# Kernel optimization log

Measured on AMD Instinct MI355X. Metric: run time of the kernel, lower is better.

The kernel has to match this reference:

```python
import jax, jax.numpy as jnp
import numpy as np

N = 32768          # nodes
E = 524288         # edges (avg degree 16)
H = 128            # hidden_features
EF = 16            # edge_features
MF = 2 * H + EF + 1  # message_features for e3, relaxed=False (distance feat = 1)


def _mlp2(x, W1, b1, W2, b2):
    # Linear -> silu -> Linear -> silu (edge_mlp)
    return jax.nn.silu(jax.nn.silu(x @ W1 + b1) @ W2 + b2)


def setup_inputs() -> dict:
    key = jax.random.key(0)
    ks = jax.random.split(key, 20)

    def glorot(k, shape):
        fan_in, fan_out = shape[0], shape[1]
        lim = np.sqrt(6.0 / (fan_in + fan_out)).astype(np.float32)
        return jax.random.uniform(k, shape, jnp.float32, -lim, lim)

    inp = {
        'src': jax.random.randint(ks[0], (E,), 0, N),
        'dst': jax.random.randint(ks[1], (E,), 0, N),
        'h': jax.random.normal(ks[2], (N, H), jnp.float32),
        'coords': jax.random.normal(ks[3], (N, 3), jnp.float32),
        'a': jax.random.normal(ks[4], (E, EF), jnp.float32),
        # coord_mlp: MF -> H -> H -> 1 (last bias-free, xavier gain 0.001)
        'W_c1': glorot(ks[5], (MF, H)), 'b_c1': jnp.zeros((H,), jnp.float32),
        'W_c2': glorot(ks[6], (H, H)),  'b_c2': jnp.zeros((H,), jnp.float32),
        'W_c3': glorot(ks[7], (H, 1)) * 0.001,
        # edge_mlp: MF -> H -> H
        'W_e1': glorot(ks[8], (MF, H)), 'b_e1': jnp.zeros((H,), jnp.float32),
        'W_e2': glorot(ks[9], (H, H)),  'b_e2': jnp.zeros((H,), jnp.float32),
        # att_mlp: H -> 1
        'W_att': glorot(ks[10], (H, 1)), 'b_att': jnp.zeros((1,), jnp.float32),
        # node_mlp: 2H -> H -> H
        'W_n1': glorot(ks[11], (2 * H, H)), 'b_n1': jnp.zeros((H,), jnp.float32),
        'W_n2': glorot(ks[12], (H, H)),     'b_n2': jnp.zeros((H,), jnp.float32),
    }
    return inp


def reference(src, dst, h, coords, a,
              W_c1, b_c1, W_c2, b_c2, W_c3,
              W_e1, b_e1, W_e2, b_e2,
              W_att, b_att,
              W_n1, b_n1, W_n2, b_n2):
    # --- edge gather + distance features (equivariance='e3', relaxed=False) ---
    srcs_x = coords[src]                      # [E, 3]
    dsts_x = coords[dst]
    diffs = srcs_x - dsts_x                   # [E, 3]
    radials = jnp.sum(diffs * diffs, axis=-1, keepdims=True)  # [E, 1]

    f = jnp.concatenate([h[src], h[dst], radials, a], axis=-1)  # [E, MF]

    # --- coord messages ---
    c = jax.nn.silu(f @ W_c1 + b_c1)
    c = jax.nn.silu(c @ W_c2 + b_c2)
    scale = c @ W_c3                          # [E, 1]
    msg_x = scale * diffs / (jnp.sqrt(radials + 1e-05) + 1.0)   # [E, 3]

    # --- hidden messages with attention gating ---
    msg_h = _mlp2(f, W_e1, b_e1, W_e2, b_e2)  # [E, H]
    att = jax.nn.sigmoid(msg_h @ W_att + b_att)  # [E, 1]
    msg_h = att * msg_h

    # --- scatter-sum aggregation at destination nodes ---
    x_agg = jax.ops.segment_sum(msg_x, dst, num_segments=N)  # [N, 3]
    h_agg = jax.ops.segment_sum(msg_h, dst, num_segments=N)  # [N, H]

    coords_out = coords + x_agg
    nh = jax.nn.silu(jnp.concatenate([h, h_agg], axis=-1) @ W_n1 + b_n1) @ W_n2 + b_n2
    h_out = h + nh
    return (h_out, coords_out)
```

## Files before the change

### kernel.cpp

```cpp
#include <hip/hip_runtime.h>
#include <math.h>

#define HD   128
#define EFD  16
#define MT   64
#define LPA  264
#define LPC  136

#define W1SZ (128 * 288)
#define W2SZ (128 * 128)
#define O_WE1 (W1SZ)
#define O_WC2 (2 * W1SZ)
#define O_WE2 (2 * W1SZ + W2SZ)
#define O_WN1 (2 * W1SZ + 2 * W2SZ)
#define O_WN2 (2 * W1SZ + 2 * W2SZ + 128 * 256)
#define WS_ELEMS (O_WN2 + W2SZ)

#define B_H16   ((size_t)0)
#define B_WPAN  ((size_t)8388608)
#define B_CNT   ((size_t)8699904)
#define B_OFS   ((size_t)8830976)
#define B_SRCP  ((size_t)8962048)
#define B_DSTP  ((size_t)11059200)
#define B_A16   ((size_t)13156352)

typedef __attribute__((ext_vector_type(8))) short short8;
typedef __attribute__((ext_vector_type(4))) float f32x4;

__device__ __forceinline__ unsigned short f2bf(float x) {
    __bf16 b = (__bf16)x;
    unsigned short u;
    __builtin_memcpy(&u, &b, 2);
    return u;
}
__device__ __forceinline__ float bf2f(unsigned short u) {
    union { unsigned u; float f; } v; v.u = ((unsigned)u) << 16;
    return v.f;
}
__device__ __forceinline__ float sigm_f(float x) {
    return __builtin_amdgcn_rcpf(1.f + __expf(-x));
}
__device__ __forceinline__ float silu_f(float x) { return x * sigm_f(x); }
__device__ __forceinline__ unsigned pack2(float a, float b) {
    return (unsigned)f2bf(a) | ((unsigned)f2bf(b) << 16);
}

__device__ __forceinline__ void frag_l1(int idx, const float* __restrict__ W,
                                        const float* __restrict__ bias,
                                        unsigned short* __restrict__ out)
{
    const int j = idx & 7, lane = (idx >> 3) & 63, blk = idx >> 9;
    const int kc = blk % 9, n = blk / 9;
    const int k = kc * 32 + (lane >> 4) * 8 + j;
    const int c = n * 16 + (lane & 15);
    float v = 0.f;
    if (k < 256) v = W[k * HD + c];
    else if (k < 272) v = W[(k + 1) * HD + c];
    else if (k == 272) v = W[256 * HD + c];
    else if (k == 273) v = bias[c];
    out[idx] = f2bf(v);
}
__device__ __forceinline__ void frag_sq(int idx, const float* __restrict__ W,
                                        int nkc, unsigned short* __restrict__ out)
{
    const int j = idx & 7, lane = (idx >> 3) & 63, blk = idx >> 9;
    const int kc = blk % nkc, n = blk / nkc;
    const int k = kc * 32 + (lane >> 4) * 8 + j;
    const int c = n * 16 + (lane & 15);
    out[idx] = f2bf(W[k * HD + c]);
}

__global__ __launch_bounds__(256) void fused_prep(
    const float* __restrict__ h, unsigned short* __restrict__ h16,
    const float* __restrict__ Wc1, const float* __restrict__ bc1,
    const float* __restrict__ We1, const float* __restrict__ be1,
    const float* __restrict__ Wc2, const float* __restrict__ We2,
    const float* __restrict__ Wn1, const float* __restrict__ Wn2,
    unsigned short* __restrict__ ws,
    const int* __restrict__ dst, unsigned* __restrict__ cnt,
    int nConv, int nPrep, int E)
{
    const int bid = blockIdx.x, tid = threadIdx.x;
    if (bid < nConv) {
        const int i = bid * 256 + tid;
        const float4 v = ((const float4*)h)[i];
        union { unsigned short us[4]; uint2 u2; } p;
        p.us[0] = f2bf(v.x); p.us[1] = f2bf(v.y);
        p.us[2] = f2bf(v.z); p.us[3] = f2bf(v.w);
        ((uint2*)h16)[i] = p.u2;
        return;
    }
    if (bid < nConv + nPrep) {
        int idx = (bid - nConv) * 256 + tid;
        if (idx < W1SZ)            { frag_l1(idx, Wc1, bc1, ws);            return; }
        idx -= W1SZ;
        if (idx < W1SZ)            { frag_l1(idx, We1, be1, ws + O_WE1);    return; }
        idx -= W1SZ;
        if (idx < W2SZ)            { frag_sq(idx, Wc2, 4, ws + O_WC2);      return; }
        idx -= W2SZ;
        if (idx < W2SZ)            { frag_sq(idx, We2, 4, ws + O_WE2);      return; }
        idx -= W2SZ;
        if (idx < 128 * 256)       { frag_sq(idx, Wn1, 8, ws + O_WN1);      return; }
        idx -= 128 * 256;
        if (idx < W2SZ)            { frag_sq(idx, Wn2, 4, ws + O_WN2); }
        return;
    }
    const int i = (bid - nConv - nPrep) * 256 + tid;
    if (i < E) atomicAdd(&cnt[dst[i]], 1u);
}

__global__ __launch_bounds__(1024) void scan32k(const unsigned* __restrict__ cnt,
                                                unsigned* __restrict__ ofs)
{
    __shared__ unsigned wsum[16];
    __shared__ unsigned carry_s;
    const int tid = threadIdx.x, lane = tid & 63, w = tid >> 6;
    if (tid == 0) carry_s = 0;
    __syncthreads();
    for (int c = 0; c < 32; ++c) {
        const unsigned x = cnt[c * 1024 + tid];
        unsigned v = x;
        #pragma unroll
        for (int off = 1; off < 64; off <<= 1) {
            unsigned t = __shfl_up(v, off);
            if (lane >= off) v += t;
        }
        if (lane == 63) wsum[w] = v;
        __syncthreads();
        if (tid < 16) {
            unsigned s = wsum[tid];
            #pragma unroll
            for (int off = 1; off < 16; off <<= 1) {
                unsigned t = __shfl_up(s, off);
                if (tid >= off) s += t;
            }
            wsum[tid] = s;
        }
        __syncthreads();
        const unsigned carry = carry_s;
        const unsigned woff = (w == 0) ? 0u : wsum[w - 1];
        ofs[c * 1024 + tid] = carry + woff + v - x;
        __syncthreads();
        if (tid == 0) carry_s = carry + wsum[15];
        __syncthreads();
    }
}

__global__ __launch_bounds__(256) void scatter_perm(
    const int* __restrict__ src, const int* __restrict__ dst,
    const float* __restrict__ a, unsigned* __restrict__ ofs,
    int* __restrict__ srcp, int* __restrict__ dstp,
    unsigned short* __restrict__ a16p, int E)
{
    const int i = blockIdx.x * 256 + threadIdx.x;
    if (i >= E) return;
    const int d = dst[i];
    const unsigned pos = atomicAdd(&ofs[d], 1u);
    srcp[pos] = src[i];
    dstp[pos] = d;
    const float* ar = a + (size_t)i * EFD;
    union { unsigned short us[8]; short8 v; } p0, p1;
    #pragma unroll
    for (int t = 0; t < 8; ++t) { p0.us[t] = f2bf(ar[t]); p1.us[t] = f2bf(ar[8 + t]); }
    short8* dstv = (short8*)(a16p + (size_t)pos * EFD);
    dstv[0] = p0.v; dstv[1] = p1.v;
}

__global__ __launch_bounds__(256, 4) void edge_kernel(
    const int* __restrict__ srcp, const int* __restrict__ dstp,
    const unsigned short* __restrict__ a16p,
    const float* __restrict__ coords, const unsigned short* __restrict__ h16,
    const float* __restrict__ bc2, const float* __restrict__ Wc3,
    const float* __restrict__ be2,
    const float* __restrict__ Watt, const float* __restrict__ batt,
    const unsigned short* __restrict__ wpan,
    float* __restrict__ out_h, float* __restrict__ out_x)
{
    __shared__ __align__(16) unsigned short csh_c[MT][LPC];
    __shared__ __align__(16) unsigned short csh_e[MT][LPC];
    __shared__ float diff_s[MT][3];
    __shared__ float rinv_s[MT];
    __shared__ float rad_s[MT];
    __shared__ float sc_part[4][MT];
    __shared__ float pa_part[4][MT];
    __shared__ float att_s[MT];
    __shared__ float sc_s[MT];
    __shared__ int   src_s[MT], dst_s[MT];
    __shared__ short run_start[MT + 1];
    __shared__ int   nruns_s;

    const int tid = threadIdx.x;
    const int e0  = blockIdx.x * MT;

    if (tid < MT) {
        const int s = srcp[e0 + tid], d = dstp[e0 + tid];
        src_s[tid] = s; dst_s[tid] = d;
        const float dx = coords[(size_t)s*3+0] - coords[(size_t)d*3+0];
        const float dy = coords[(size_t)s*3+1] - coords[(size_t)d*3+1];
        const float dz = coords[(size_t)s*3+2] - coords[(size_t)d*3+2];
        diff_s[tid][0] = dx; diff_s[tid][1] = dy; diff_s[tid][2] = dz;
        const float rad = dx*dx + dy*dy + dz*dz;
        rad_s[tid]  = rad;
        rinv_s[tid] = __builtin_amdgcn_rcpf(sqrtf(rad + 1e-5f) + 1.f);
    }
    __syncthreads();

    if (tid < 64) {
        const bool st = (tid == 0) || (dst_s[tid] != dst_s[tid - 1]);
        unsigned long long m = __ballot(st);
        if (tid == 0) {
            int nr = 0;
            while (m) { run_start[nr++] = (short)__builtin_ctzll(m); m &= m - 1; }
            run_start[nr] = MT;
            nruns_s = nr;
        }
    }

    const int lane = tid & 63;
    const int w    = tid >> 6;
    const int w2   = w * 2;
    const int col  = lane & 15;
    const int kg   = lane >> 4;

    const unsigned short* Wc1p = wpan            + lane * 8;
    const unsigned short* We1p = wpan + O_WE1    + lane * 8;
    const unsigned short* Wc2p = wpan + O_WC2    + lane * 8;
    const unsigned short* We2p = wpan + O_WE2    + lane * 8;

    const unsigned short* hs[4];
    const unsigned short* hd[4];
    #pragma unroll
    for (int et = 0; et < 4; ++et) {
        const int r = et * 16 + col;
        hs[et] = h16 + (size_t)src_s[r] * HD;
        hd[et] = h16 + (size_t)dst_s[r] * HD;
    }

    const f32x4 zero = {0.f, 0.f, 0.f, 0.f};
    const short8 zf  = {0,0,0,0,0,0,0,0};
    f32x4 ac[2][4], ae[2][4];

    #pragma unroll
    for (int m = 0; m < 2; ++m)
        #pragma unroll
        for (int et = 0; et < 4; ++et) { ac[m][et] = zero; ae[m][et] = zero; }

    #pragma unroll
    for (int kc = 0; kc < 9; ++kc) {
        short8 df[4];
        #pragma unroll
        for (int et = 0; et < 4; ++et) {
            if (kc < 4)       df[et] = *(const short8*)(hs[et] + kc * 32 + kg * 8);
            else if (kc < 8)  df[et] = *(const short8*)(hd[et] + (kc - 4) * 32 + kg * 8);
            else if (kg < 2)  df[et] = *(const short8*)(a16p + (size_t)(e0 + et*16 + col) * EFD + kg * 8);
            else if (kg == 2) {
                df[et] = zf;
                df[et][0] = (short)f2bf(rad_s[et*16 + col]);
                df[et][1] = (short)0x3F80;
            } else df[et] = zf;
        }
        #pragma unroll
        for (int m = 0; m < 2; ++m) {
            const short8 wc = *(const short8*)&Wc1p[((w2 + m) * 9 + kc) << 9];
            const short8 we = *(const short8*)&We1p[((w2 + m) * 9 + kc) << 9];
            #pragma unroll
            for (int et = 0; et < 4; ++et) {
                ac[m][et] = __builtin_amdgcn_mfma_f32_16x16x32_bf16(wc, df[et], ac[m][et], 0, 0, 0);
                ae[m][et] = __builtin_amdgcn_mfma_f32_16x16x32_bf16(we, df[et], ae[m][et], 0, 0, 0);
            }
        }
    }
    #pragma unroll
    for (int m = 0; m < 2; ++m)
        #pragma unroll
        for (int et = 0; et < 4; ++et) {
            const int row = et * 16 + col;
            const int hw  = w * 32 + m * 16 + kg * 4;
            uint2 vc, ve;
            vc.x = pack2(silu_f(ac[m][et][0]), silu_f(ac[m][et][1]));
            vc.y = pack2(silu_f(ac[m][et][2]), silu_f(ac[m][et][3]));
            ve.x = pack2(silu_f(ae[m][et][0]), silu_f(ae[m][et][1]));
            ve.y = pack2(silu_f(ae[m][et][2]), silu_f(ae[m][et][3]));
            *(uint2*)&csh_c[row][hw] = vc;
            *(uint2*)&csh_e[row][hw] = ve;
        }
    __syncthreads();

    #pragma unroll
    for (int m = 0; m < 2; ++m)
        #pragma unroll
        for (int et = 0; et < 4; ++et) { ac[m][et] = zero; ae[m][et] = zero; }

    #pragma unroll
    for (int kc = 0; kc < 4; ++kc) {
        short8 dc[4], de[4];
        #pragma unroll
        for (int et = 0; et < 4; ++et) {
            const int row = et * 16 + col;
            dc[et] = *(const short8*)&csh_c[row][kc * 32 + kg * 8];
            de[et] = *(const short8*)&csh_e[row][kc * 32 + kg * 8];
        }
        #pragma unroll
        for (int m = 0; m < 2; ++m) {
            const short8 wc = *(const short8*)&Wc2p[((w2 + m) * 4 + kc) << 9];
            const short8 we = *(const short8*)&We2p[((w2 + m) * 4 + kc) << 9];
            #pragma unroll
            for (int et = 0; et < 4; ++et) {
                ac[m][et] = __builtin_amdgcn_mfma_f32_16x16x32_bf16(wc, dc[et], ac[m][et], 0, 0, 0);
                ae[m][et] = __builtin_amdgcn_mfma_f32_16x16x32_bf16(we, de[et], ae[m][et], 0, 0, 0);
            }
        }
    }

    {
        float sc[4] = {0.f, 0.f, 0.f, 0.f};
        #pragma unroll
        for (int m = 0; m < 2; ++m)
            #pragma unroll
            for (int i = 0; i < 4; ++i) {
                const int hw = w * 32 + m * 16 + kg * 4 + i;
                const float b = bc2[hw], w3 = Wc3[hw];
                #pragma unroll
                for (int et = 0; et < 4; ++et)
                    sc[et] += silu_f(ac[m][et][i] + b) * w3;
            }
        #pragma unroll
        for (int et = 0; et < 4; ++et) {
            sc[et] += __shfl_xor(sc[et], 16);
            sc[et] += __shfl_xor(sc[et], 32);
        }
        if (kg == 0) {
            #pragma unroll
            for (int et = 0; et < 4; ++et)
                sc_part[w][et * 16 + col] = sc[et];
        }
    }
    __syncthreads();

    {
        float pa[4] = {0.f, 0.f, 0.f, 0.f};
        #pragma unroll
        for (int m = 0; m < 2; ++m)
            #pragma unroll
            for (int et = 0; et < 4; ++et) {
                const int row = et * 16 + col;
                const int hw  = w * 32 + m * 16 + kg * 4;
                const float v0 = silu_f(ae[m][et][0] + be2[hw]);
                const float v1 = silu_f(ae[m][et][1] + be2[hw+1]);
                const float v2 = silu_f(ae[m][et][2] + be2[hw+2]);
                const float v3 = silu_f(ae[m][et][3] + be2[hw+3]);
                pa[et] += v0 * Watt[hw] + v1 * Watt[hw+1]
                        + v2 * Watt[hw+2] + v3 * Watt[hw+3];
                uint2 ve;
                ve.x = pack2(v0, v1);
                ve.y = pack2(v2, v3);
                *(uint2*)&csh_e[row][hw] = ve;
            }
        #pragma unroll
        for (int et = 0; et < 4; ++et) {
            pa[et] += __shfl_xor(pa[et], 16);
            pa[et] += __shfl_xor(pa[et], 32);
        }
        if (kg == 0) {
            #pragma unroll
            for (int et = 0; et < 4; ++et)
                pa_part[w][et * 16 + col] = pa[et];
        }
    }
    __syncthreads();

    if (tid < MT) {
        att_s[tid] = sigm_f(pa_part[0][tid] + pa_part[1][tid] +
                            pa_part[2][tid] + pa_part[3][tid] + batt[0]);
        sc_s[tid]  = (sc_part[0][tid] + sc_part[1][tid] +
                      sc_part[2][tid] + sc_part[3][tid]) * rinv_s[tid];
    }
    __syncthreads();

    {
        const int nr    = nruns_s;
        const int colx2 = tid & 63;
        for (int r = tid >> 6; r < nr; r += 4) {
            const int s0 = run_start[r], s1 = run_start[r + 1];
            float sum0 = 0.f, sum1 = 0.f;
            for (int e = s0; e < s1; ++e) {
                const unsigned uv = *(const unsigned*)&csh_e[e][colx2 * 2];
                const float at = att_s[e];
                sum0 += bf2f((unsigned short)uv) * at;
                sum1 += bf2f((unsigned short)(uv >> 16)) * at;
            }
            const int drow = dst_s[s0];
            float* op = out_h + (size_t)drow * HD + colx2 * 2;
            atomicAdd(op,     sum0);
            atomicAdd(op + 1, sum1);
            if (colx2 < 2) {
                float sx0 = 0.f, sx1 = 0.f;
                for (int e = s0; e < s1; ++e) {
                    const float s = sc_s[e];
                    sx0 += s * diff_s[e][colx2 * 2];
                    if (colx2 == 0) sx1 += s * diff_s[e][1];
                }
                atomicAdd(&out_x[(size_t)drow * 3 + colx2 * 2], sx0);
                if (colx2 == 0) atomicAdd(&out_x[(size_t)drow * 3 + 1], sx1);
            }
        }
    }
}

__global__ __launch_bounds__(256) void node_kernel(
    const float* __restrict__ h, const float* __restrict__ coords,
    const float* __restrict__ bn1, const float* __restrict__ bn2,
    const unsigned short* __restrict__ wpan,
    float* __restrict__ out_h, float* __restrict__ out_x)
{
    __shared__ __align__(16) unsigned short ash[MT][LPA];
    __shared__ __align__(16) unsigned short csh[MT][LPC];

    const int tid = threadIdx.x;
    const int n0  = blockIdx.x * MT;

    #pragma unroll
    for (int it = 0; it < 16; ++it) {
        const int idx = it * 256 + tid;
        const int e = idx >> 6, q = idx & 63;
        const float* base = (q < 32)
            ? h     + (size_t)(n0 + e) * HD + q * 4
            : out_h + (size_t)(n0 + e) * HD + (q - 32) * 4;
        const float4 v = *(const float4*)base;
        union { unsigned short us[4]; uint2 u2; } p;
        p.us[0] = f2bf(v.x); p.us[1] = f2bf(v.y);
        p.us[2] = f2bf(v.z); p.us[3] = f2bf(v.w);
        *(uint2*)&ash[e][q * 4] = p.u2;
    }
    __syncthreads();

    if (tid < MT * 3) {
        const int n = tid / 3, d = tid % 3;
        const size_t gi = (size_t)(n0 + n) * 3 + d;
        out_x[gi] += coords[gi];
    }

    const int lane = tid & 63;
    const int w    = tid >> 6;
    const int er0  = w * 16;
    const int col  = lane & 15;
    const int kg   = lane >> 4;

    const unsigned short* Wn1p = wpan + O_WN1 + lane * 8;
    const unsigned short* Wn2p = wpan + O_WN2 + lane * 8;

    const f32x4 zero = {0.f, 0.f, 0.f, 0.f};
    f32x4 acc[8];

    #pragma unroll
    for (int n = 0; n < 8; ++n) acc[n] = zero;
    #pragma unroll
    for (int kc = 0; kc < 8; ++kc) {
        const short8 af = *(const short8*)&ash[er0 + col][kc * 32 + kg * 8];
        #pragma unroll
        for (int n = 0; n < 8; ++n) {
            const short8 bf = *(const short8*)&Wn1p[(n * 8 + kc) << 9];
            acc[n] = __builtin_amdgcn_mfma_f32_16x16x32_bf16(af, bf, acc[n], 0, 0, 0);
        }
    }
    #pragma unroll
    for (int n = 0; n < 8; ++n) {
        const float b = bn1[n*16 + col];
        #pragma unroll
        for (int i = 0; i < 4; ++i)
            csh[er0 + kg*4 + i][n*16 + col] = f2bf(silu_f(acc[n][i] + b));
    }
    __syncthreads();
    #pragma unroll
    for (int n = 0; n < 8; ++n) acc[n] = zero;
    #pragma unroll
    for (int kc = 0; kc < 4; ++kc) {
        const short8 af = *(const short8*)&csh[er0 + col][kc * 32 + kg * 8];
        #pragma unroll
        for (int n = 0; n < 8; ++n) {
            const short8 bf = *(const short8*)&Wn2p[(n * 4 + kc) << 9];
            acc[n] = __builtin_amdgcn_mfma_f32_16x16x32_bf16(af, bf, acc[n], 0, 0, 0);
        }
    }
    #pragma unroll
    for (int i = 0; i < 4; ++i) {
        const int node = n0 + er0 + kg*4 + i;
        const float* hr   = h     + (size_t)node * HD;
        float*       orow = out_h + (size_t)node * HD;
        #pragma unroll
        for (int n = 0; n < 8; ++n) {
            const int f = n*16 + col;
            orow[f] = hr[f] + acc[n][i] + bn2[f];
        }
    }
}

extern "C" void kernel_launch(void* const* d_in, const int* in_sizes, int n_in,
                              void* d_out, int out_size, void* d_ws, size_t ws_size,
                              hipStream_t stream)
{
    const int*   src    = (const int*)  d_in[0];
    const int*   dst    = (const int*)  d_in[1];
    const float* h      = (const float*)d_in[2];
    const float* coords = (const float*)d_in[3];
    const float* a      = (const float*)d_in[4];
    const float* Wc1    = (const float*)d_in[5];
    const float* bc1    = (const float*)d_in[6];
    const float* Wc2    = (const float*)d_in[7];
    const float* bc2    = (const float*)d_in[8];
    const float* Wc3    = (const float*)d_in[9];
    const float* We1    = (const float*)d_in[10];
    const float* be1    = (const float*)d_in[11];
    const float* We2    = (const float*)d_in[12];
    const float* be2    = (const float*)d_in[13];
    const float* Watt   = (const float*)d_in[14];
    const float* batt   = (const float*)d_in[15];
    const float* Wn1    = (const float*)d_in[16];
    const float* bn1    = (const float*)d_in[17];
    const float* Wn2    = (const float*)d_in[18];
    const float* bn2    = (const float*)d_in[19];

    const int E = in_sizes[0];
    const int N = in_sizes[2] / HD;

    float* out_h = (float*)d_out;
    float* out_x = out_h + (size_t)N * HD;

    char* wsb = (char*)d_ws;
    unsigned short* h16  = (unsigned short*)(wsb + B_H16);
    unsigned short* wpan = (unsigned short*)(wsb + B_WPAN);
    unsigned*       cnt  = (unsigned*)      (wsb + B_CNT);
    unsigned*       ofs  = (unsigned*)      (wsb + B_OFS);
    int*            srcp = (int*)           (wsb + B_SRCP);
    int*            dstp = (int*)           (wsb + B_DSTP);
    unsigned short* a16p = (unsigned short*)(wsb + B_A16);

    hipMemsetAsync(d_out, 0, (size_t)out_size * sizeof(float), stream);
    hipMemsetAsync(cnt, 0, (size_t)N * sizeof(unsigned), stream);

    const int nConv = (N * HD / 4) / 256;
    const int nPrep = WS_ELEMS / 256;
    const int nHist = (E + 255) / 256;

    fused_prep<<<dim3(nConv + nPrep + nHist), dim3(256), 0, stream>>>(
        h, h16, Wc1, bc1, We1, be1, Wc2, We2, Wn1, Wn2, wpan,
        dst, cnt, nConv, nPrep, E);

    scan32k<<<dim3(1), dim3(1024), 0, stream>>>(cnt, ofs);
    scatter_perm<<<dim3((E + 255) / 256), dim3(256), 0, stream>>>(
        src, dst, a, ofs, srcp, dstp, a16p, E);

    edge_kernel<<<dim3(E / MT), dim3(256), 0, stream>>>(
        srcp, dstp, a16p, coords, h16,
        bc2, Wc3, be2, Watt, batt,
        wpan, out_h, out_x);

    node_kernel<<<dim3(N / MT), dim3(256), 0, stream>>>(
        h, coords, bn1, bn2, wpan, out_h, out_x);
}
```

Measured before the change: 324.3 us.

## Precompute per-node first-layer projections and gather them per edge

Splits the first edge/coord MLP layer algebraically: h[src]@W_src and h[dst]@W_dst are computed once per node in a new node_pre kernel and stored as bf16 tables. The edge kernel then gathers and adds these partial sums instead of running eight K-chunks of MFMA on gathered h rows, keeping only the radial/edge-feature chunk. The scatter kernel now writes an edge index permutation instead of a converted a16 copy, and the edge kernel reads a directly. This trades edge-side matmul FLOPs for four extra bf16 gathers per edge. It also adds bf16 rounding of the partial sums and a larger workspace.

```diff
diff --git a/kernel.cpp b/kernel.cpp
--- a/kernel.cpp
+++ b/kernel.cpp
@@ -16,13 +16,16 @@
 #define O_WN2 (2 * W1SZ + 2 * W2SZ + 128 * 256)
 #define WS_ELEMS (O_WN2 + W2SZ)
 
-#define B_H16   ((size_t)0)
-#define B_WPAN  ((size_t)8388608)
-#define B_CNT   ((size_t)8699904)
-#define B_OFS   ((size_t)8830976)
-#define B_SRCP  ((size_t)8962048)
-#define B_DSTP  ((size_t)11059200)
-#define B_A16   ((size_t)13156352)
+#define B_PSC   ((size_t)0)
+#define B_PDC   ((size_t)8388608)
+#define B_PSE   ((size_t)16777216)
+#define B_PDE   ((size_t)25165824)
+#define B_WPAN  ((size_t)33554432)
+#define B_CNT   ((size_t)33865728)
+#define B_OFS   ((size_t)33996800)
+#define B_SRCP  ((size_t)34127872)
+#define B_DSTP  ((size_t)36225024)
+#define B_EIDX  ((size_t)38322176)
 
 typedef __attribute__((ext_vector_type(8))) short short8;
 typedef __attribute__((ext_vector_type(4))) float f32x4;
@@ -36,6 +39,12 @@
 __device__ __forceinline__ float bf2f(unsigned short u) {
     union { unsigned u; float f; } v; v.u = ((unsigned)u) << 16;
     return v.f;
+}
+__device__ __forceinline__ float bfl(unsigned u) {
+    union { unsigned u; float f; } v; v.u = u << 16; return v.f;
+}
+__device__ __forceinline__ float bfh(unsigned u) {
+    union { unsigned u; float f; } v; v.u = u & 0xffff0000u; return v.f;
 }
 __device__ __forceinline__ float sigm_f(float x) {
     return __builtin_amdgcn_rcpf(1.f + __expf(-x));
@@ -71,27 +80,17 @@
 }
 
 __global__ __launch_bounds__(256) void fused_prep(
-    const float* __restrict__ h, unsigned short* __restrict__ h16,
     const float* __restrict__ Wc1, const float* __restrict__ bc1,
     const float* __restrict__ We1, const float* __restrict__ be1,
     const float* __restrict__ Wc2, const float* __restrict__ We2,
     const float* __restrict__ Wn1, const float* __restrict__ Wn2,
     unsigned short* __restrict__ ws,
     const int* __restrict__ dst, unsigned* __restrict__ cnt,
-    int nConv, int nPrep, int E)
+    int nPrep, int E)
 {
     const int bid = blockIdx.x, tid = threadIdx.x;
-    if (bid < nConv) {
-        const int i = bid * 256 + tid;
-        const float4 v = ((const float4*)h)[i];
-        union { unsigned short us[4]; uint2 u2; } p;
-        p.us[0] = f2bf(v.x); p.us[1] = f2bf(v.y);
-        p.us[2] = f2bf(v.z); p.us[3] = f2bf(v.w);
-        ((uint2*)h16)[i] = p.u2;
-        return;
-    }
-    if (bid < nConv + nPrep) {
-        int idx = (bid - nConv) * 256 + tid;
+    if (bid < nPrep) {
+        int idx = bid * 256 + tid;
         if (idx < W1SZ)            { frag_l1(idx, Wc1, bc1, ws);            return; }
         idx -= W1SZ;
         if (idx < W1SZ)            { frag_l1(idx, We1, be1, ws + O_WE1);    return; }
@@ -105,8 +104,82 @@
         if (idx < W2SZ)            { frag_sq(idx, Wn2, 4, ws + O_WN2); }
         return;
     }
-    const int i = (bid - nConv - nPrep) * 256 + tid;
+    const int i = (bid - nPrep) * 256 + tid;
     if (i < E) atomicAdd(&cnt[dst[i]], 1u);
+}
+
+__device__ __forceinline__ void pre_pass(
+    const unsigned short* __restrict__ panelp,
+    const unsigned short* __restrict__ hsh,
+    unsigned short* __restrict__ Ps, unsigned short* __restrict__ Pd,
+    int n0, int w2, int w, int col, int kg)
+{
+    const f32x4 zero = {0.f, 0.f, 0.f, 0.f};
+    f32x4 as_[2][4], ad_[2][4];
+    #pragma unroll
+    for (int m = 0; m < 2; ++m)
+        #pragma unroll
+        for (int et = 0; et < 4; ++et) { as_[m][et] = zero; ad_[m][et] = zero; }
+    #pragma unroll
+    for (int kc = 0; kc < 4; ++kc) {
+        short8 bf[4];
+        #pragma unroll
+        for (int et = 0; et < 4; ++et)
+            bf[et] = *(const short8*)&hsh[(et*16 + col) * LPC + kc * 32 + kg * 8];
+        #pragma unroll
+        for (int m = 0; m < 2; ++m) {
+            const short8 As = *(const short8*)&panelp[((w2 + m) * 9 + kc) << 9];
+            const short8 Ad = *(const short8*)&panelp[((w2 + m) * 9 + kc + 4) << 9];
+            #pragma unroll
+            for (int et = 0; et < 4; ++et) {
+                as_[m][et] = __builtin_amdgcn_mfma_f32_16x16x32_bf16(As, bf[et], as_[m][et], 0, 0, 0);
+                ad_[m][et] = __builtin_amdgcn_mfma_f32_16x16x32_bf16(Ad, bf[et], ad_[m][et], 0, 0, 0);
+            }
+        }
+    }
+    #pragma unroll
+    for (int m = 0; m < 2; ++m)
+        #pragma unroll
+        for (int et = 0; et < 4; ++et) {
+            const size_t row = (size_t)(n0 + et * 16 + col) * HD;
+            const int hw = w * 32 + m * 16 + kg * 4;
+            uint2 vs, vd;
+            vs.x = pack2(as_[m][et][0], as_[m][et][1]);
+            vs.y = pack2(as_[m][et][2], as_[m][et][3]);
+            vd.x = pack2(ad_[m][et][0], ad_[m][et][1]);
+            vd.y = pack2(ad_[m][et][2], ad_[m][et][3]);
+            *(uint2*)(Ps + row + hw) = vs;
+            *(uint2*)(Pd + row + hw) = vd;
+        }
+}
+
+__global__ __launch_bounds__(256) void node_pre(
+    const float* __restrict__ h, const unsigned short* __restrict__ wpan,
+    unsigned short* __restrict__ Psc, unsigned short* __restrict__ Pdc,
+    unsigned short* __restrict__ Pse, unsigned short* __restrict__ Pde)
+{
+    __shared__ __align__(16) unsigned short hsh[MT][LPC];
+    const int tid = threadIdx.x;
+    const int n0  = blockIdx.x * MT;
+
+    #pragma unroll
+    for (int it = 0; it < 8; ++it) {
+        const int idx = it * 256 + tid;
+        const int r = idx >> 5, q = idx & 31;
+        const float4 v = *(const float4*)(h + (size_t)(n0 + r) * HD + q * 4);
+        uint2 p; p.x = pack2(v.x, v.y); p.y = pack2(v.z, v.w);
+        *(uint2*)&hsh[r][q * 4] = p;
+    }
+    __syncthreads();
+
+    const int lane = tid & 63;
+    const int w    = tid >> 6;
+    const int w2   = w * 2;
+    const int col  = lane & 15;
+    const int kg   = lane >> 4;
+
+    pre_pass(wpan + lane * 8,         &hsh[0][0], Psc, Pdc, n0, w2, w, col, kg);
+    pre_pass(wpan + O_WE1 + lane * 8, &hsh[0][0], Pse, Pde, n0, w2, w, col, kg);
 }
 
 __global__ __launch_bounds__(1024) void scan32k(const unsigned* __restrict__ cnt,
@@ -148,9 +221,9 @@
 
 __global__ __launch_bounds__(256) void scatter_perm(
     const int* __restrict__ src, const int* __restrict__ dst,
-    const float* __restrict__ a, unsigned* __restrict__ ofs,
+    unsigned* __restrict__ ofs,
     int* __restrict__ srcp, int* __restrict__ dstp,
-    unsigned short* __restrict__ a16p, int E)
+    int* __restrict__ eidx, int E)
 {
     const int i = blockIdx.x * 256 + threadIdx.x;
     if (i >= E) return;
@@ -158,18 +231,15 @@
     const unsigned pos = atomicAdd(&ofs[d], 1u);
     srcp[pos] = src[i];
     dstp[pos] = d;
-    const float* ar = a + (size_t)i * EFD;
-    union { unsigned short us[8]; short8 v; } p0, p1;
-    #pragma unroll
-    for (int t = 0; t < 8; ++t) { p0.us[t] = f2bf(ar[t]); p1.us[t] = f2bf(ar[8 + t]); }
-    short8* dstv = (short8*)(a16p + (size_t)pos * EFD);
-    dstv[0] = p0.v; dstv[1] = p1.v;
+    eidx[pos] = i;
 }
 
 __global__ __launch_bounds__(256, 4) void edge_kernel(
     const int* __restrict__ srcp, const int* __restrict__ dstp,
-    const unsigned short* __restrict__ a16p,
-    const float* __restrict__ coords, const unsigned short* __restrict__ h16,
+    const int* __restrict__ eidx, const float* __restrict__ a,
+    const float* __restrict__ coords,
+    const unsigned short* __restrict__ Psc, const unsigned short* __restrict__ Pdc,
+    const unsigned short* __restrict__ Pse, const unsigned short* __restrict__ Pde,
     const float* __restrict__ bc2, const float* __restrict__ Wc3,
     const float* __restrict__ be2,
     const float* __restrict__ Watt, const float* __restrict__ batt,
@@ -179,13 +249,13 @@
     __shared__ __align__(16) unsigned short csh_c[MT][LPC];
     __shared__ __align__(16) unsigned short csh_e[MT][LPC];
     __shared__ float diff_s[MT][3];
+    __shared__ float rad_s[MT];
     __shared__ float rinv_s[MT];
-    __shared__ float rad_s[MT];
     __shared__ float sc_part[4][MT];
     __shared__ float pa_part[4][MT];
     __shared__ float att_s[MT];
     __shared__ float sc_s[MT];
-    __shared__ int   src_s[MT], dst_s[MT];
+    __shared__ int   src_s[MT], dst_s[MT], eid_s[MT];
     __shared__ short run_start[MT + 1];
     __shared__ int   nruns_s;
 
@@ -195,6 +265,7 @@
     if (tid < MT) {
         const int s = srcp[e0 + tid], d = dstp[e0 + tid];
         src_s[tid] = s; dst_s[tid] = d;
+        eid_s[tid] = eidx[e0 + tid];
         const float dx = coords[(size_t)s*3+0] - coords[(size_t)d*3+0];
         const float dy = coords[(size_t)s*3+1] - coords[(size_t)d*3+1];
         const float dz = coords[(size_t)s*3+2] - coords[(size_t)d*3+2];
@@ -227,42 +298,60 @@
     const unsigned short* Wc2p = wpan + O_WC2    + lane * 8;
     const unsigned short* We2p = wpan + O_WE2    + lane * 8;
 
-    const unsigned short* hs[4];
-    const unsigned short* hd[4];
+    unsigned po_s[4], po_d[4];
     #pragma unroll
     for (int et = 0; et < 4; ++et) {
         const int r = et * 16 + col;
-        hs[et] = h16 + (size_t)src_s[r] * HD;
-        hd[et] = h16 + (size_t)dst_s[r] * HD;
-    }
-
-    const f32x4 zero = {0.f, 0.f, 0.f, 0.f};
-    const short8 zf  = {0,0,0,0,0,0,0,0};
+        const unsigned wk = (unsigned)(w * 64 + kg * 8);
+        po_s[et] = (unsigned)src_s[r] * 256u + wk;
+        po_d[et] = (unsigned)dst_s[r] * 256u + wk;
+    }
+
+    const short8 zf = {0,0,0,0,0,0,0,0};
     f32x4 ac[2][4], ae[2][4];
 
     #pragma unroll
     for (int m = 0; m < 2; ++m)
         #pragma unroll
-        for (int et = 0; et < 4; ++et) { ac[m][et] = zero; ae[m][et] = zero; }
-
-    #pragma unroll
-    for (int kc = 0; kc < 9; ++kc) {
+        for (int et = 0; et < 4; ++et) {
+            const uint2 sc_ = *(const uint2*)((const char*)Psc + po_s[et] + m * 32);
+            const uint2 dc_ = *(const uint2*)((const char*)Pdc + po_d[et] + m * 32);
+            const uint2 se_ = *(const uint2*)((const char*)Pse + po_s[et] + m * 32);
+            const uint2 de_ = *(const uint2*)((const char*)Pde + po_d[et] + m * 32);
+            ac[m][et][0] = bfl(sc_.x) + bfl(dc_.x);
+            ac[m][et][1] = bfh(sc_.x) + bfh(dc_.x);
+            ac[m][et][2] = bfl(sc_.y) + bfl(dc_.y);
+            ac[m][et][3] = bfh(sc_.y) + bfh(dc_.y);
+            ae[m][et][0] = bfl(se_.x) + bfl(de_.x);
+            ae[m][et][1] = bfh(se_.x) + bfh(de_.x);
+            ae[m][et][2] = bfl(se_.y) + bfl(de_.y);
+            ae[m][et][3] = bfh(se_.y) + bfh(de_.y);
+        }
+    {
         short8 df[4];
         #pragma unroll
         for (int et = 0; et < 4; ++et) {
-            if (kc < 4)       df[et] = *(const short8*)(hs[et] + kc * 32 + kg * 8);
-            else if (kc < 8)  df[et] = *(const short8*)(hd[et] + (kc - 4) * 32 + kg * 8);
-            else if (kg < 2)  df[et] = *(const short8*)(a16p + (size_t)(e0 + et*16 + col) * EFD + kg * 8);
-            else if (kg == 2) {
-                df[et] = zf;
-                df[et][0] = (short)f2bf(rad_s[et*16 + col]);
-                df[et][1] = (short)0x3F80;
+            if (kg < 2) {
+                const int oe = eid_s[et * 16 + col];
+                const float4 a0 = *(const float4*)(a + (size_t)oe * EFD + kg * 8);
+                const float4 a1 = *(const float4*)(a + (size_t)oe * EFD + kg * 8 + 4);
+                short8 v;
+                v[0] = (short)f2bf(a0.x); v[1] = (short)f2bf(a0.y);
+                v[2] = (short)f2bf(a0.z); v[3] = (short)f2bf(a0.w);
+                v[4] = (short)f2bf(a1.x); v[5] = (short)f2bf(a1.y);
+                v[6] = (short)f2bf(a1.z); v[7] = (short)f2bf(a1.w);
+                df[et] = v;
+            } else if (kg == 2) {
+                short8 v = zf;
+                v[0] = (short)f2bf(rad_s[et * 16 + col]);
+                v[1] = (short)0x3F80;
+                df[et] = v;
             } else df[et] = zf;
         }
         #pragma unroll
         for (int m = 0; m < 2; ++m) {
-            const short8 wc = *(const short8*)&Wc1p[((w2 + m) * 9 + kc) << 9];
-            const short8 we = *(const short8*)&We1p[((w2 + m) * 9 + kc) << 9];
+            const short8 wc = *(const short8*)&Wc1p[((w2 + m) * 9 + 8) << 9];
+            const short8 we = *(const short8*)&We1p[((w2 + m) * 9 + 8) << 9];
             #pragma unroll
             for (int et = 0; et < 4; ++et) {
                 ac[m][et] = __builtin_amdgcn_mfma_f32_16x16x32_bf16(wc, df[et], ac[m][et], 0, 0, 0);
@@ -286,6 +375,7 @@
         }
     __syncthreads();
 
+    const f32x4 zero = {0.f, 0.f, 0.f, 0.f};
     #pragma unroll
     for (int m = 0; m < 2; ++m)
         #pragma unroll
@@ -386,8 +476,8 @@
             for (int e = s0; e < s1; ++e) {
                 const unsigned uv = *(const unsigned*)&csh_e[e][colx2 * 2];
                 const float at = att_s[e];
-                sum0 += bf2f((unsigned short)uv) * at;
-                sum1 += bf2f((unsigned short)(uv >> 16)) * at;
+                sum0 += bfl(uv) * at;
+                sum1 += bfh(uv) * at;
             }
             const int drow = dst_s[s0];
             float* op = out_h + (size_t)drow * HD + colx2 * 2;
@@ -527,31 +617,37 @@
     float* out_x = out_h + (size_t)N * HD;
 
     char* wsb = (char*)d_ws;
-    unsigned short* h16  = (unsigned short*)(wsb + B_H16);
+    unsigned short* Psc  = (unsigned short*)(wsb + B_PSC);
+    unsigned short* Pdc  = (unsigned short*)(wsb + B_PDC);
+    unsigned short* Pse  = (unsigned short*)(wsb + B_PSE);
+    unsigned short* Pde  = (unsigned short*)(wsb + B_PDE);
     unsigned short* wpan = (unsigned short*)(wsb + B_WPAN);
     unsigned*       cnt  = (unsigned*)      (wsb + B_CNT);
     unsigned*       ofs  = (unsigned*)      (wsb + B_OFS);
     int*            srcp = (int*)           (wsb + B_SRCP);
     int*            dstp = (int*)           (wsb + B_DSTP);
-    unsigned short* a16p = (unsigned short*)(wsb + B_A16);
+    int*            eidx = (int*)           (wsb + B_EIDX);
 
     hipMemsetAsync(d_out, 0, (size_t)out_size * sizeof(float), stream);
     hipMemsetAsync(cnt, 0, (size_t)N * sizeof(unsigned), stream);
 
-    const int nConv = (N * HD / 4) / 256;
     const int nPrep = WS_ELEMS / 256;
     const int nHist = (E + 255) / 256;
 
-    fused_prep<<<dim3(nConv + nPrep + nHist), dim3(256), 0, stream>>>(
-        h, h16, Wc1, bc1, We1, be1, Wc2, We2, Wn1, Wn2, wpan,
-        dst, cnt, nConv, nPrep, E);
+    fused_prep<<<dim3(nPrep + nHist), dim3(256), 0, stream>>>(
+        Wc1, bc1, We1, be1, Wc2, We2, Wn1, Wn2, wpan,
+        dst, cnt, nPrep, E);
+
+    node_pre<<<dim3(N / MT), dim3(256), 0, stream>>>(
+        h, wpan, Psc, Pdc, Pse, Pde);
 
     scan32k<<<dim3(1), dim3(1024), 0, stream>>>(cnt, ofs);
     scatter_perm<<<dim3((E + 255) / 256), dim3(256), 0, stream>>>(
-        src, dst, a, ofs, srcp, dstp, a16p, E);
+        src, dst, ofs, srcp, dstp, eidx, E);
 
     edge_kernel<<<dim3(E / MT), dim3(256), 0, stream>>>(
-        srcp, dstp, a16p, coords, h16,
+        srcp, dstp, eidx, a, coords,
+        Psc, Pdc, Pse, Pde,
         bc2, Wc3, be2, Watt, batt,
         wpan, out_h, out_x);
 
```

Result: no change. 318.3 us (-1.8%).
